# Performance work log

Measured on AMD Instinct MI355X. Metric: run time of the kernel, lower is better.

Reference implementation:

```python
import jax, jax.numpy as jnp
import numpy as np
import math

EMBED_DIM = 256
NUM_HEADS = 8
NUM_LEVELS = 4
NUM_POINTS = 4
HEAD_DIM = EMBED_DIM // NUM_HEADS
SPATIAL_SHAPES = np.array([[100, 100], [50, 50], [25, 25], [13, 13]], dtype=np.int64)
LEN_V = int((SPATIAL_SHAPES[:, 0] * SPATIAL_SHAPES[:, 1]).sum())  # 13294
BS, LEN_Q = 8, 1024


def _grid_sample_bilinear(img, grid):
    """img: [N, C, H, W]; grid: [N, Hg, Wg, 2] in [-1,1].
    bilinear, padding_mode='zeros', align_corners=False. Returns [N, Hg, Wg, C]."""
    N, C, H, W = img.shape
    x = (grid[..., 0] + 1.0) * (W * 0.5) - 0.5
    y = (grid[..., 1] + 1.0) * (H * 0.5) - 0.5
    x0 = jnp.floor(x)
    y0 = jnp.floor(y)
    x1 = x0 + 1.0
    y1 = y0 + 1.0
    wx1 = x - x0
    wx0 = 1.0 - wx1
    wy1 = y - y0
    wy0 = 1.0 - wy1
    b = jnp.arange(N)[:, None, None]

    def gather(yi, xi):
        valid = (yi >= 0) & (yi <= H - 1) & (xi >= 0) & (xi <= W - 1)
        yc = jnp.clip(yi, 0, H - 1).astype(jnp.int32)
        xc = jnp.clip(xi, 0, W - 1).astype(jnp.int32)
        v = img[b, :, yc, xc]  # [N, Hg, Wg, C]
        return v * valid[..., None].astype(img.dtype)

    out = (gather(y0, x0) * (wy0 * wx0)[..., None]
           + gather(y0, x1) * (wy0 * wx1)[..., None]
           + gather(y1, x0) * (wy1 * wx0)[..., None]
           + gather(y1, x1) * (wy1 * wx1)[..., None])
    return out


def _offset_bias_init():
    # Faithful to _reset_parameters: per-head directional grid init for offsets bias.
    thetas = np.arange(NUM_HEADS, dtype=np.float32) * (2.0 * math.pi / NUM_HEADS)
    g = np.stack([np.cos(thetas), np.sin(thetas)], -1)
    g = g / np.abs(g).max(-1, keepdims=True)
    g = np.tile(g.reshape(NUM_HEADS, 1, 1, 2), (1, NUM_LEVELS, NUM_POINTS, 1))
    g = g * np.arange(1, NUM_POINTS + 1, dtype=np.float32).reshape(1, 1, -1, 1)
    return jnp.asarray(g.reshape(-1))


def setup_inputs() -> dict:
    key = jax.random.key(0)
    ks = jax.random.split(key, 8)
    TP = NUM_HEADS * NUM_LEVELS * NUM_POINTS  # 128

    def xavier(k, fan_in, fan_out):
        lim = math.sqrt(6.0 / (fan_in + fan_out))
        return jax.random.uniform(k, (fan_in, fan_out), jnp.float32, -lim, lim)

    return {
        "query": jax.random.normal(ks[0], (BS, LEN_Q, EMBED_DIM), jnp.float32),
        "reference_points": jax.random.uniform(ks[1], (BS, LEN_Q, NUM_LEVELS, 2), jnp.float32),
        "value": jax.random.normal(ks[2], (BS, LEN_V, EMBED_DIM), jnp.float32),
        "value_spatial_shapes": SPATIAL_SHAPES,
        # small random weights (instead of the zero-init) so the math paths are exercised
        "so_w": 0.01 * jax.random.normal(ks[3], (EMBED_DIM, TP * 2), jnp.float32),
        "so_b": _offset_bias_init(),
        "aw_w": 0.01 * jax.random.normal(ks[4], (EMBED_DIM, TP), jnp.float32),
        "aw_b": jnp.zeros((TP,), jnp.float32),
        "vp_w": xavier(ks[5], EMBED_DIM, EMBED_DIM),
        "vp_b": jnp.zeros((EMBED_DIM,), jnp.float32),
        "op_w": xavier(ks[6], EMBED_DIM, EMBED_DIM),
        "op_b": jnp.zeros((EMBED_DIM,), jnp.float32),
    }


def reference(query, reference_points, value, value_spatial_shapes,
              so_w, so_b, aw_w, aw_b, vp_w, vp_b, op_w, op_b):
    shapes = np.asarray(value_spatial_shapes)  # static python ints
    bs, len_q, D = query.shape
    H, L, P, hd = NUM_HEADS, NUM_LEVELS, NUM_POINTS, HEAD_DIM

    v = value @ vp_w + vp_b                              # [bs, len_v, D]
    v = v.reshape(bs, -1, H, hd)                         # [bs, len_v, H, hd]

    so = (query @ so_w + so_b).reshape(bs, len_q, H, L, P, 2)
    aw = (query @ aw_w + aw_b).reshape(bs, len_q, H, L * P)
    aw = jax.nn.softmax(aw, axis=-1).reshape(bs, len_q, H, L, P)

    # reference_points last dim == 2 branch: normalize offsets by (w, h) per level
    norm = jnp.asarray(shapes[:, ::-1].copy(), dtype=query.dtype).reshape(1, 1, 1, L, 1, 2)
    loc = reference_points.reshape(bs, len_q, 1, L, 1, 2) + so / norm
    grids = 2.0 * loc - 1.0                              # [bs, len_q, H, L, P, 2]
    grids = grids.transpose(0, 2, 1, 3, 4, 5).reshape(bs * H, len_q, L, P, 2)

    samples = []
    start = 0
    for lvl in range(L):
        h, w = int(shapes[lvl, 0]), int(shapes[lvl, 1])
        vl = v[:, start:start + h * w]                   # [bs, hw, H, hd]
        start += h * w
        img = vl.transpose(0, 2, 3, 1).reshape(bs * H, hd, h, w)
        s = _grid_sample_bilinear(img, grids[:, :, lvl])  # [bs*H, len_q, P, hd]
        samples.append(s)
    samp = jnp.stack(samples, axis=2)                    # [bs*H, len_q, L, P, hd]

    w_ = aw.transpose(0, 2, 1, 3, 4).reshape(bs * H, len_q, L, P)
    out = jnp.einsum('nqlpd,nqlp->nqd', samp, w_)        # [bs*H, len_q, hd]
    out = out.reshape(bs, H, len_q, hd).transpose(0, 2, 1, 3).reshape(bs, len_q, D)
    return out @ op_w + op_b
```

## Files before the change

kernel.cpp:

```cpp
#include <hip/hip_runtime.h>
#include <math.h>

#define BSZ 8
#define LQ  1024
#define LV  13294
#define NH  8
#define HD  32
#define VM  (BSZ * LV)

typedef __attribute__((ext_vector_type(8))) short bf16x8;
typedef __attribute__((ext_vector_type(8))) unsigned short u16x8;
typedef __attribute__((ext_vector_type(4))) float f32x4;

__device__ static inline unsigned short f2bf(float f) {
    unsigned int u = __float_as_uint(f);
    unsigned int r = (u + 0x7FFFu + ((u >> 16) & 1u)) >> 16;
    return (unsigned short)r;
}
__device__ static inline float bf2f(unsigned short s) {
    return __uint_as_float(((unsigned int)s) << 16);
}

__global__ __launch_bounds__(256) void wconv_kernel(
    const float* __restrict__ w, unsigned short* __restrict__ wT)
{
    const int n = blockIdx.x;
    const int k = threadIdx.x;
    wT[n * 256 + k] = f2bf(w[k * 256 + n]);
}

__global__ __launch_bounds__(256, 2) void vproj_mfma_kernel(
    const float* __restrict__ A,
    const unsigned short* __restrict__ wT,
    const float* __restrict__ bias,
    unsigned short* __restrict__ v)
{
    __shared__ __align__(16) unsigned short Asb[64 * 256];

    const int tid  = threadIdx.x;
    const int w    = tid >> 6;
    const int lane = tid & 63;
    const int mrow = lane & 15;
    const int quad = lane >> 4;
    const int m0   = blockIdx.x * 64;

    bf16x8 wf[4][8];
#pragma unroll
    for (int j = 0; j < 4; ++j) {
        const int n = w * 64 + j * 16 + mrow;
#pragma unroll
        for (int kc = 0; kc < 8; ++kc)
            wf[j][kc] = *(const bf16x8*)(const void*)(wT + (size_t)n * 256 + kc * 32 + quad * 8);
    }
    float bj[4];
#pragma unroll
    for (int j = 0; j < 4; ++j) bj[j] = bias[w * 64 + j * 16 + mrow];

    {
        const int m  = tid >> 2;
        const int kq = tid & 3;
        const int gm = m0 + m;
        const float* ap = A + (size_t)gm * 256 + kq * 64;
        unsigned short* lrow = &Asb[m * 256];
#pragma unroll
        for (int u = 0; u < 8; ++u) {
            const int c  = kq * 8 + u;
            const int cp = c ^ (m & 31);
            u16x8 b8 = (u16x8)0;
            if (gm < VM) {
                const float4 f0 = *(const float4*)(ap + u * 8);
                const float4 f1 = *(const float4*)(ap + u * 8 + 4);
                b8[0] = f2bf(f0.x); b8[1] = f2bf(f0.y);
                b8[2] = f2bf(f0.z); b8[3] = f2bf(f0.w);
                b8[4] = f2bf(f1.x); b8[5] = f2bf(f1.y);
                b8[6] = f2bf(f1.z); b8[7] = f2bf(f1.w);
            }
            *(u16x8*)(lrow + cp * 8) = b8;
        }
    }
    __syncthreads();

    f32x4 acc[4][4];
#pragma unroll
    for (int i = 0; i < 4; ++i)
#pragma unroll
        for (int j = 0; j < 4; ++j) acc[i][j] = (f32x4)0.f;

#pragma unroll
    for (int kc = 0; kc < 8; ++kc) {
        bf16x8 af[4];
#pragma unroll
        for (int i = 0; i < 4; ++i) {
            const int mr = i * 16 + mrow;
            const int c  = kc * 4 + quad;
            const int cp = c ^ (mr & 31);
            af[i] = *(const bf16x8*)(const void*)&Asb[mr * 256 + cp * 8];
        }
#pragma unroll
        for (int i = 0; i < 4; ++i)
#pragma unroll
            for (int j = 0; j < 4; ++j)
                acc[i][j] = __builtin_amdgcn_mfma_f32_16x16x32_bf16(
                    af[i], wf[j][kc], acc[i][j], 0, 0, 0);
    }

#pragma unroll
    for (int i = 0; i < 4; ++i) {
#pragma unroll
        for (int r = 0; r < 4; ++r) {
            const int gm = m0 + i * 16 + quad * 4 + r;
            if (gm >= VM) continue;
            const unsigned int b   = (unsigned int)gm / (unsigned int)LV;
            const unsigned int pix = (unsigned int)gm - b * (unsigned int)LV;
#pragma unroll
            for (int j = 0; j < 4; ++j) {
                const int gn = w * 64 + j * 16 + mrow;
                const int h = gn >> 5, c = gn & 31;
                v[(((size_t)(b * NH + h)) * LV + pix) * HD + c] =
                    f2bf(acc[i][j][r] + bj[j]);
            }
        }
    }
}

__global__ __launch_bounds__(256) void qproj_kernel(
    const float* __restrict__ A,
    const float* __restrict__ so_w, const float* __restrict__ so_b,
    const float* __restrict__ aw_w, const float* __restrict__ aw_b,
    float* __restrict__ so_raw, float* __restrict__ aw_raw)
{
    __shared__ float As[16][68];
    __shared__ float Ws[16][68];

    const int tid = threadIdx.x;
    const int tx = tid & 15, ty = tid >> 4;
    const int m0 = blockIdx.y * 64;
    const int n0g = blockIdx.x * 64;

    const float* W; const float* bias; float* C; int N, n0;
    if (n0g < 256) { W = so_w; bias = so_b; C = so_raw; N = 256; n0 = n0g; }
    else           { W = aw_w; bias = aw_b; C = aw_raw; N = 128; n0 = n0g - 256; }

    const int ra = tid >> 2;
    const int ka = (tid & 3) << 2;
    const int rw = tid >> 4;
    const int cw = (tid & 15) << 2;

    float acc[4][4];
#pragma unroll
    for (int i = 0; i < 4; ++i)
#pragma unroll
        for (int j = 0; j < 4; ++j) acc[i][j] = 0.f;

    for (int k0 = 0; k0 < 256; k0 += 16) {
        const float4 av = *(const float4*)(A + (size_t)(m0 + ra) * 256 + (k0 + ka));
        As[ka + 0][ra] = av.x;
        As[ka + 1][ra] = av.y;
        As[ka + 2][ra] = av.z;
        As[ka + 3][ra] = av.w;
        *(float4*)&Ws[rw][cw] =
            *(const float4*)(W + (size_t)(k0 + rw) * N + (n0 + cw));
        __syncthreads();
#pragma unroll
        for (int k = 0; k < 16; ++k) {
            const float4 a4 = *(const float4*)&As[k][ty << 2];
            const float4 b4 = *(const float4*)&Ws[k][tx << 2];
            const float aa[4] = {a4.x, a4.y, a4.z, a4.w};
            const float bb[4] = {b4.x, b4.y, b4.z, b4.w};
#pragma unroll
            for (int i = 0; i < 4; ++i)
#pragma unroll
                for (int j = 0; j < 4; ++j)
                    acc[i][j] = fmaf(aa[i], bb[j], acc[i][j]);
        }
        __syncthreads();
    }

#pragma unroll
    for (int i = 0; i < 4; ++i) {
        const int row = m0 + (ty << 2) + i;
#pragma unroll
        for (int j = 0; j < 4; ++j) {
            const int col = n0 + (tx << 2) + j;
            C[(size_t)row * N + col] = acc[i][j] + bias[col];
        }
    }
}

__global__ __launch_bounds__(256) void sgemm_kernel(
    const float* __restrict__ A, const float* __restrict__ W,
    const float* __restrict__ bias, float* __restrict__ C)
{
    __shared__ float As[16][68];
    __shared__ float Ws[16][68];

    const int tid = threadIdx.x;
    const int tx = tid & 15, ty = tid >> 4;
    const int m0 = blockIdx.y * 64;
    const int n0 = blockIdx.x * 64;

    const int ra = tid >> 2;
    const int ka = (tid & 3) << 2;
    const int rw = tid >> 4;
    const int cw = (tid & 15) << 2;

    float acc[4][4];
#pragma unroll
    for (int i = 0; i < 4; ++i)
#pragma unroll
        for (int j = 0; j < 4; ++j) acc[i][j] = 0.f;

    for (int k0 = 0; k0 < 256; k0 += 16) {
        const float4 av = *(const float4*)(A + (size_t)(m0 + ra) * 256 + (k0 + ka));
        As[ka + 0][ra] = av.x;
        As[ka + 1][ra] = av.y;
        As[ka + 2][ra] = av.z;
        As[ka + 3][ra] = av.w;
        *(float4*)&Ws[rw][cw] =
            *(const float4*)(W + (size_t)(k0 + rw) * 256 + (n0 + cw));
        __syncthreads();
#pragma unroll
        for (int k = 0; k < 16; ++k) {
            const float4 a4 = *(const float4*)&As[k][ty << 2];
            const float4 b4 = *(const float4*)&Ws[k][tx << 2];
            const float aa[4] = {a4.x, a4.y, a4.z, a4.w};
            const float bb[4] = {b4.x, b4.y, b4.z, b4.w};
#pragma unroll
            for (int i = 0; i < 4; ++i)
#pragma unroll
                for (int j = 0; j < 4; ++j)
                    acc[i][j] = fmaf(aa[i], bb[j], acc[i][j]);
        }
        __syncthreads();
    }

#pragma unroll
    for (int i = 0; i < 4; ++i) {
        const int row = m0 + (ty << 2) + i;
#pragma unroll
        for (int j = 0; j < 4; ++j) {
            const int col = n0 + (tx << 2) + j;
            C[(size_t)row * 256 + col] = acc[i][j] + bias[col];
        }
    }
}

__global__ __launch_bounds__(256) void sample_kernel(
    const unsigned short* __restrict__ v,
    const float* __restrict__ so_raw,
    const float* __restrict__ aw_raw,
    const float* __restrict__ refp,
    float* __restrict__ out_head)
{
    __shared__ __align__(16) float wts[512][4];
    __shared__ __align__(16) int   offs[512][4];

    const int blk   = blockIdx.x;
    const int xcd   = blk & 7;
    const int j     = blk >> 3;
    const int bh    = xcd * 8 + (j >> 5);
    const int chunk = j & 31;
    const int h     = bh & 7;
    const int b     = bh >> 3;

    const int t = threadIdx.x;

#pragma unroll
    for (int rep = 0; rep < 2; ++rep) {
        const int s  = t + rep * 256;
        const int qq = s >> 4;
        const int pt = s & 15;
        const int l  = pt >> 2;
        const int p  = pt & 3;
        const int rq = b * LQ + chunk * 32 + qq;

        const int Wl = (l == 0) ? 100 : (l == 1) ? 50 : (l == 2) ? 25 : 13;
        const int st = (l == 0) ? 0 : (l == 1) ? 10000 : (l == 2) ? 12500 : 13125;
        const float invW = (l == 0) ? 0.01f : (l == 1) ? 0.02f : (l == 2) ? 0.04f
                                            : (1.0f / 13.0f);
        const float fw = (float)Wl;

        const float logit = aw_raw[rq * 128 + h * 16 + pt];
        float mx = logit;
#pragma unroll
        for (int d = 1; d < 16; d <<= 1) mx = fmaxf(mx, __shfl_xor(mx, d, 16));
        const float e = expf(logit - mx);
        float sm = e;
#pragma unroll
        for (int d = 1; d < 16; d <<= 1) sm += __shfl_xor(sm, d, 16);
        const float wgt = e / sm;

        const float rx = refp[((size_t)rq * 4 + l) * 2 + 0];
        const float ry = refp[((size_t)rq * 4 + l) * 2 + 1];
        const int soi  = rq * 256 + h * 32 + l * 8 + p * 2;
        const float sx = so_raw[soi];
        const float sy = so_raw[soi + 1];

        const float x = (rx + sx * invW) * fw - 0.5f;
        const float y = (ry + sy * invW) * fw - 0.5f;

        const float xf = floorf(x), yf = floorf(y);
        const int x0 = (int)xf, y0 = (int)yf;
        const float wx1 = x - xf, wx0 = 1.f - wx1;
        const float wy1 = y - yf, wy0 = 1.f - wy1;

        const float vx0 = (x0 >= 0 && x0 < Wl) ? 1.f : 0.f;
        const float vx1 = (x0 + 1 >= 0 && x0 + 1 < Wl) ? 1.f : 0.f;
        const float vy0 = (y0 >= 0 && y0 < Wl) ? 1.f : 0.f;
        const float vy1 = (y0 + 1 >= 0 && y0 + 1 < Wl) ? 1.f : 0.f;

        const int xc0 = min(max(x0, 0), Wl - 1);
        const int xc1 = min(max(x0 + 1, 0), Wl - 1);
        const int yc0 = min(max(y0, 0), Wl - 1);
        const int yc1 = min(max(y0 + 1, 0), Wl - 1);

        const int row0 = st + yc0 * Wl;
        const int row1 = st + yc1 * Wl;

        wts[s][0] = wgt * wy0 * wx0 * vy0 * vx0;
        wts[s][1] = wgt * wy0 * wx1 * vy0 * vx1;
        wts[s][2] = wgt * wy1 * wx0 * vy1 * vx0;
        wts[s][3] = wgt * wy1 * wx1 * vy1 * vx1;
        offs[s][0] = (row0 + xc0) * HD;
        offs[s][1] = (row0 + xc1) * HD;
        offs[s][2] = (row1 + xc0) * HD;
        offs[s][3] = (row1 + xc1) * HD;
    }
    __syncthreads();

    const int qq = t >> 3;
    const int ln = t & 7;
    const unsigned short* vb = v + (size_t)bh * (LV * HD) + ln * 4;

    float a0 = 0.f, a1 = 0.f, a2 = 0.f, a3 = 0.f;

#pragma unroll 4
    for (int pt = 0; pt < 16; ++pt) {
        const int s = qq * 16 + pt;
        const float4 w4 = *(const float4*)&wts[s][0];
        const int4   o4 = *(const int4*)&offs[s][0];

        const ushort4 u0 = *(const ushort4*)(vb + o4.x);
        const ushort4 u1 = *(const ushort4*)(vb + o4.y);
        const ushort4 u2 = *(const ushort4*)(vb + o4.z);
        const ushort4 u3 = *(const ushort4*)(vb + o4.w);

        a0 = fmaf(w4.x, bf2f(u0.x), a0);
        a1 = fmaf(w4.x, bf2f(u0.y), a1);
        a2 = fmaf(w4.x, bf2f(u0.z), a2);
        a3 = fmaf(w4.x, bf2f(u0.w), a3);
        a0 = fmaf(w4.y, bf2f(u1.x), a0);
        a1 = fmaf(w4.y, bf2f(u1.y), a1);
        a2 = fmaf(w4.y, bf2f(u1.z), a2);
        a3 = fmaf(w4.y, bf2f(u1.w), a3);
        a0 = fmaf(w4.z, bf2f(u2.x), a0);
        a1 = fmaf(w4.z, bf2f(u2.y), a1);
        a2 = fmaf(w4.z, bf2f(u2.z), a2);
        a3 = fmaf(w4.z, bf2f(u2.w), a3);
        a0 = fmaf(w4.w, bf2f(u3.x), a0);
        a1 = fmaf(w4.w, bf2f(u3.y), a1);
        a2 = fmaf(w4.w, bf2f(u3.z), a2);
        a3 = fmaf(w4.w, bf2f(u3.w), a3);
    }

    const int rq = b * LQ + chunk * 32 + qq;
    float4 o; o.x = a0; o.y = a1; o.z = a2; o.w = a3;
    *(float4*)(out_head + (size_t)rq * 256 + (h << 5) + (ln << 2)) = o;
}

extern "C" void kernel_launch(void* const* d_in, const int* in_sizes, int n_in,
                              void* d_out, int out_size, void* d_ws, size_t ws_size,
                              hipStream_t stream)
{
    const float* query = (const float*)d_in[0];
    const float* refp  = (const float*)d_in[1];
    const float* value = (const float*)d_in[2];
    const float* so_w  = (const float*)d_in[4];
    const float* so_b  = (const float*)d_in[5];
    const float* aw_w  = (const float*)d_in[6];
    const float* aw_b  = (const float*)d_in[7];
    const float* vp_w  = (const float*)d_in[8];
    const float* vp_b  = (const float*)d_in[9];
    const float* op_w  = (const float*)d_in[10];
    const float* op_b  = (const float*)d_in[11];
    float* out = (float*)d_out;

    float* ws = (float*)d_ws;
    size_t off = 0;
    unsigned short* v = (unsigned short*)(ws + off);
    off += (size_t)BSZ * NH * LV * HD / 2;
    unsigned short* wT = (unsigned short*)(ws + off); off += 32768;
    float* so_raw   = ws + off; off += (size_t)BSZ * LQ * 256;
    float* aw_raw   = ws + off; off += (size_t)BSZ * LQ * 128;
    float* out_head = ws + off; off += (size_t)BSZ * LQ * 256;

    wconv_kernel<<<256, 256, 0, stream>>>(vp_w, wT);

    {
        dim3 grid((VM + 63) / 64);
        vproj_mfma_kernel<<<grid, 256, 0, stream>>>(value, wT, vp_b, v);
    }
    {
        dim3 grid(6, BSZ * LQ / 64);
        qproj_kernel<<<grid, 256, 0, stream>>>(query, so_w, so_b, aw_w, aw_b,
                                               so_raw, aw_raw);
    }
    {
        dim3 grid(BSZ * NH * (LQ / 32));
        sample_kernel<<<grid, 256, 0, stream>>>(v, so_raw, aw_raw, refp, out_head);
    }
    {
        dim3 grid(256 / 64, BSZ * LQ / 64);
        sgemm_kernel<<<grid, 256, 0, stream>>>(out_head, op_w, op_b, out);
    }
}
```

Before: 287.2 us.

## Move output projection to bf16 MFMA and stream value projection without LDS

Replaces the fp32 SIMT output-projection GEMM with a bf16 MFMA kernel, and the sampling kernel now writes its per-head output as bf16 to feed it. The value-projection kernel drops its LDS staging, reads fp32 rows directly into registers, converts them to bf16, and swaps the MFMA operands so each lane writes contiguous packed output. Both weight transposes run in a single conversion launch. The aim is to cut FP32 ALU cost and memory traffic, at the cost of extra bf16 rounding in the output path and uncoalesced-looking strided global reads in the value GEMM.

Result: slower. 340.5 us (+18.6%).

```diff
diff --git a/kernel.cpp b/kernel.cpp
--- a/kernel.cpp
+++ b/kernel.cpp
@@ -1,4 +1,5 @@
 #include <hip/hip_runtime.h>
+#include <hip/hip_bf16.h>
 #include <math.h>
 
 #define BSZ 8
@@ -9,7 +10,6 @@
 #define VM  (BSZ * LV)
 
 typedef __attribute__((ext_vector_type(8))) short bf16x8;
-typedef __attribute__((ext_vector_type(8))) unsigned short u16x8;
 typedef __attribute__((ext_vector_type(4))) float f32x4;
 
 __device__ static inline unsigned short f2bf(float f) {
@@ -20,23 +20,29 @@
 __device__ static inline float bf2f(unsigned short s) {
     return __uint_as_float(((unsigned int)s) << 16);
 }
+__device__ static inline unsigned int pk2bf(float a, float b) {
+    __hip_bfloat162 h = __float22bfloat162_rn(make_float2(a, b));
+    return *(unsigned int*)&h;
+}
+
+union BF8 { unsigned int u[4]; bf16x8 v; };
 
 __global__ __launch_bounds__(256) void wconv_kernel(
-    const float* __restrict__ w, unsigned short* __restrict__ wT)
-{
-    const int n = blockIdx.x;
+    const float* __restrict__ w0, const float* __restrict__ w1,
+    unsigned short* __restrict__ t0, unsigned short* __restrict__ t1)
+{
+    const int n = blockIdx.x & 255;
     const int k = threadIdx.x;
-    wT[n * 256 + k] = f2bf(w[k * 256 + n]);
-}
-
-__global__ __launch_bounds__(256, 2) void vproj_mfma_kernel(
+    if (blockIdx.x < 256) t0[n * 256 + k] = f2bf(w0[k * 256 + n]);
+    else                  t1[n * 256 + k] = f2bf(w1[k * 256 + n]);
+}
+
+__global__ __launch_bounds__(512, 2) void vproj_mfma_kernel(
     const float* __restrict__ A,
     const unsigned short* __restrict__ wT,
     const float* __restrict__ bias,
     unsigned short* __restrict__ v)
 {
-    __shared__ __align__(16) unsigned short Asb[64 * 256];
-
     const int tid  = threadIdx.x;
     const int w    = tid >> 6;
     const int lane = tid & 63;
@@ -44,81 +50,126 @@
     const int quad = lane >> 4;
     const int m0   = blockIdx.x * 64;
 
-    bf16x8 wf[4][8];
-#pragma unroll
-    for (int j = 0; j < 4; ++j) {
-        const int n = w * 64 + j * 16 + mrow;
+    bf16x8 wf[2][8];
+#pragma unroll
+    for (int j = 0; j < 2; ++j) {
+        const int n = w * 32 + j * 16 + mrow;
 #pragma unroll
         for (int kc = 0; kc < 8; ++kc)
             wf[j][kc] = *(const bf16x8*)(const void*)(wT + (size_t)n * 256 + kc * 32 + quad * 8);
     }
-    float bj[4];
-#pragma unroll
-    for (int j = 0; j < 4; ++j) bj[j] = bias[w * 64 + j * 16 + mrow];
-
-    {
-        const int m  = tid >> 2;
-        const int kq = tid & 3;
-        const int gm = m0 + m;
-        const float* ap = A + (size_t)gm * 256 + kq * 64;
-        unsigned short* lrow = &Asb[m * 256];
-#pragma unroll
-        for (int u = 0; u < 8; ++u) {
-            const int c  = kq * 8 + u;
-            const int cp = c ^ (m & 31);
-            u16x8 b8 = (u16x8)0;
-            if (gm < VM) {
-                const float4 f0 = *(const float4*)(ap + u * 8);
-                const float4 f1 = *(const float4*)(ap + u * 8 + 4);
-                b8[0] = f2bf(f0.x); b8[1] = f2bf(f0.y);
-                b8[2] = f2bf(f0.z); b8[3] = f2bf(f0.w);
-                b8[4] = f2bf(f1.x); b8[5] = f2bf(f1.y);
-                b8[6] = f2bf(f1.z); b8[7] = f2bf(f1.w);
-            }
-            *(u16x8*)(lrow + cp * 8) = b8;
-        }
-    }
-    __syncthreads();
-
-    f32x4 acc[4][4];
+    float4 bj[2];
+#pragma unroll
+    for (int j = 0; j < 2; ++j)
+        bj[j] = *(const float4*)(bias + w * 32 + j * 16 + quad * 4);
+
+    f32x4 acc[4][2];
 #pragma unroll
     for (int i = 0; i < 4; ++i)
 #pragma unroll
-        for (int j = 0; j < 4; ++j) acc[i][j] = (f32x4)0.f;
+        for (int j = 0; j < 2; ++j) acc[i][j] = (f32x4)0.f;
 
 #pragma unroll
     for (int kc = 0; kc < 8; ++kc) {
-        bf16x8 af[4];
+        bf16x8 vf[4];
 #pragma unroll
         for (int i = 0; i < 4; ++i) {
-            const int mr = i * 16 + mrow;
-            const int c  = kc * 4 + quad;
-            const int cp = c ^ (mr & 31);
-            af[i] = *(const bf16x8*)(const void*)&Asb[mr * 256 + cp * 8];
+            int gm = m0 + i * 16 + mrow;
+            gm = (gm < VM) ? gm : (VM - 1);
+            const float* ap = A + (size_t)gm * 256 + kc * 32 + quad * 8;
+            const float4 f0 = *(const float4*)(ap);
+            const float4 f1 = *(const float4*)(ap + 4);
+            BF8 t;
+            t.u[0] = pk2bf(f0.x, f0.y);
+            t.u[1] = pk2bf(f0.z, f0.w);
+            t.u[2] = pk2bf(f1.x, f1.y);
+            t.u[3] = pk2bf(f1.z, f1.w);
+            vf[i] = t.v;
         }
 #pragma unroll
         for (int i = 0; i < 4; ++i)
 #pragma unroll
-            for (int j = 0; j < 4; ++j)
+            for (int j = 0; j < 2; ++j)
                 acc[i][j] = __builtin_amdgcn_mfma_f32_16x16x32_bf16(
-                    af[i], wf[j][kc], acc[i][j], 0, 0, 0);
+                    wf[j][kc], vf[i], acc[i][j], 0, 0, 0);
     }
 
 #pragma unroll
     for (int i = 0; i < 4; ++i) {
-#pragma unroll
-        for (int r = 0; r < 4; ++r) {
-            const int gm = m0 + i * 16 + quad * 4 + r;
-            if (gm >= VM) continue;
-            const unsigned int b   = (unsigned int)gm / (unsigned int)LV;
-            const unsigned int pix = (unsigned int)gm - b * (unsigned int)LV;
-#pragma unroll
-            for (int j = 0; j < 4; ++j) {
-                const int gn = w * 64 + j * 16 + mrow;
-                const int h = gn >> 5, c = gn & 31;
-                v[(((size_t)(b * NH + h)) * LV + pix) * HD + c] =
-                    f2bf(acc[i][j][r] + bj[j]);
-            }
+        const int gm = m0 + i * 16 + mrow;
+        if (gm >= VM) continue;
+        const unsigned int b   = (unsigned int)gm / (unsigned int)LV;
+        const unsigned int pix = (unsigned int)gm - b * (unsigned int)LV;
+        unsigned short* vp = v + (((size_t)(b * NH + w)) * LV + pix) * HD;
+#pragma unroll
+        for (int j = 0; j < 2; ++j) {
+            uint2 o;
+            o.x = pk2bf(acc[i][j][0] + bj[j].x, acc[i][j][1] + bj[j].y);
+            o.y = pk2bf(acc[i][j][2] + bj[j].z, acc[i][j][3] + bj[j].w);
+            *(uint2*)(vp + j * 16 + quad * 4) = o;
+        }
+    }
+}
+
+__global__ __launch_bounds__(512, 2) void oproj_mfma_kernel(
+    const unsigned short* __restrict__ Ah,
+    const unsigned short* __restrict__ opT,
+    const float* __restrict__ bias,
+    float* __restrict__ out)
+{
+    const int tid  = threadIdx.x;
+    const int w    = tid >> 6;
+    const int lane = tid & 63;
+    const int mrow = lane & 15;
+    const int quad = lane >> 4;
+    const int m0   = blockIdx.x * 32;
+
+    bf16x8 wf[2][8];
+#pragma unroll
+    for (int j = 0; j < 2; ++j) {
+        const int n = w * 32 + j * 16 + mrow;
+#pragma unroll
+        for (int kc = 0; kc < 8; ++kc)
+            wf[j][kc] = *(const bf16x8*)(const void*)(opT + (size_t)n * 256 + kc * 32 + quad * 8);
+    }
+    float4 bj[2];
+#pragma unroll
+    for (int j = 0; j < 2; ++j)
+        bj[j] = *(const float4*)(bias + w * 32 + j * 16 + quad * 4);
+
+    f32x4 acc[2][2];
+#pragma unroll
+    for (int i = 0; i < 2; ++i)
+#pragma unroll
+        for (int j = 0; j < 2; ++j) acc[i][j] = (f32x4)0.f;
+
+#pragma unroll
+    for (int kc = 0; kc < 8; ++kc) {
+        bf16x8 af[2];
+#pragma unroll
+        for (int i = 0; i < 2; ++i) {
+            const int gm = m0 + i * 16 + mrow;
+            af[i] = *(const bf16x8*)(const void*)(Ah + (size_t)gm * 256 + kc * 32 + quad * 8);
+        }
+#pragma unroll
+        for (int i = 0; i < 2; ++i)
+#pragma unroll
+            for (int j = 0; j < 2; ++j)
+                acc[i][j] = __builtin_amdgcn_mfma_f32_16x16x32_bf16(
+                    wf[j][kc], af[i], acc[i][j], 0, 0, 0);
+    }
+
+#pragma unroll
+    for (int i = 0; i < 2; ++i) {
+        const int gm = m0 + i * 16 + mrow;
+#pragma unroll
+        for (int j = 0; j < 2; ++j) {
+            float4 o;
+            o.x = acc[i][j][0] + bj[j].x;
+            o.y = acc[i][j][1] + bj[j].y;
+            o.z = acc[i][j][2] + bj[j].z;
+            o.w = acc[i][j][3] + bj[j].w;
+            *(float4*)(out + (size_t)gm * 256 + w * 32 + j * 16 + quad * 4) = o;
         }
     }
 }
@@ -187,70 +238,12 @@
     }
 }
 
-__global__ __launch_bounds__(256) void sgemm_kernel(
-    const float* __restrict__ A, const float* __restrict__ W,
-    const float* __restrict__ bias, float* __restrict__ C)
-{
-    __shared__ float As[16][68];
-    __shared__ float Ws[16][68];
-
-    const int tid = threadIdx.x;
-    const int tx = tid & 15, ty = tid >> 4;
-    const int m0 = blockIdx.y * 64;
-    const int n0 = blockIdx.x * 64;
-
-    const int ra = tid >> 2;
-    const int ka = (tid & 3) << 2;
-    const int rw = tid >> 4;
-    const int cw = (tid & 15) << 2;
-
-    float acc[4][4];
-#pragma unroll
-    for (int i = 0; i < 4; ++i)
-#pragma unroll
-        for (int j = 0; j < 4; ++j) acc[i][j] = 0.f;
-
-    for (int k0 = 0; k0 < 256; k0 += 16) {
-        const float4 av = *(const float4*)(A + (size_t)(m0 + ra) * 256 + (k0 + ka));
-        As[ka + 0][ra] = av.x;
-        As[ka + 1][ra] = av.y;
-        As[ka + 2][ra] = av.z;
-        As[ka + 3][ra] = av.w;
-        *(float4*)&Ws[rw][cw] =
-            *(const float4*)(W + (size_t)(k0 + rw) * 256 + (n0 + cw));
-        __syncthreads();
-#pragma unroll
-        for (int k = 0; k < 16; ++k) {
-            const float4 a4 = *(const float4*)&As[k][ty << 2];
-            const float4 b4 = *(const float4*)&Ws[k][tx << 2];
-            const float aa[4] = {a4.x, a4.y, a4.z, a4.w};
-            const float bb[4] = {b4.x, b4.y, b4.z, b4.w};
-#pragma unroll
-            for (int i = 0; i < 4; ++i)
-#pragma unroll
-                for (int j = 0; j < 4; ++j)
-                    acc[i][j] = fmaf(aa[i], bb[j], acc[i][j]);
-        }
-        __syncthreads();
-    }
-
-#pragma unroll
-    for (int i = 0; i < 4; ++i) {
-        const int row = m0 + (ty << 2) + i;
-#pragma unroll
-        for (int j = 0; j < 4; ++j) {
-            const int col = n0 + (tx << 2) + j;
-            C[(size_t)row * 256 + col] = acc[i][j] + bias[col];
-        }
-    }
-}
-
 __global__ __launch_bounds__(256) void sample_kernel(
     const unsigned short* __restrict__ v,
     const float* __restrict__ so_raw,
     const float* __restrict__ aw_raw,
     const float* __restrict__ refp,
-    float* __restrict__ out_head)
+    unsigned short* __restrict__ out_head)
 {
     __shared__ __align__(16) float wts[512][4];
     __shared__ __align__(16) int   offs[512][4];
@@ -364,8 +357,10 @@
     }
 
     const int rq = b * LQ + chunk * 32 + qq;
-    float4 o; o.x = a0; o.y = a1; o.z = a2; o.w = a3;
-    *(float4*)(out_head + (size_t)rq * 256 + (h << 5) + (ln << 2)) = o;
+    uint2 o;
+    o.x = pk2bf(a0, a1);
+    o.y = pk2bf(a2, a3);
+    *(uint2*)(out_head + (size_t)rq * 256 + (h << 5) + (ln << 2)) = o;
 }
 
 extern "C" void kernel_launch(void* const* d_in, const int* in_sizes, int n_in,
@@ -389,28 +384,24 @@
     size_t off = 0;
     unsigned short* v = (unsigned short*)(ws + off);
     off += (size_t)BSZ * NH * LV * HD / 2;
-    unsigned short* wT = (unsigned short*)(ws + off); off += 32768;
-    float* so_raw   = ws + off; off += (size_t)BSZ * LQ * 256;
-    float* aw_raw   = ws + off; off += (size_t)BSZ * LQ * 128;
-    float* out_head = ws + off; off += (size_t)BSZ * LQ * 256;
-
-    wconv_kernel<<<256, 256, 0, stream>>>(vp_w, wT);
-
-    {
-        dim3 grid((VM + 63) / 64);
-        vproj_mfma_kernel<<<grid, 256, 0, stream>>>(value, wT, vp_b, v);
-    }
+    unsigned short* wTv = (unsigned short*)(ws + off); off += 32768;
+    unsigned short* wTo = (unsigned short*)(ws + off); off += 32768;
+    float* so_raw = ws + off; off += (size_t)BSZ * LQ * 256;
+    float* aw_raw = ws + off; off += (size_t)BSZ * LQ * 128;
+    unsigned short* out_head = (unsigned short*)(ws + off);
+    off += (size_t)BSZ * LQ * 256 / 2;
+
+    wconv_kernel<<<512, 256, 0, stream>>>(vp_w, op_w, wTv, wTo);
+
+    vproj_mfma_kernel<<<(VM + 63) / 64, 512, 0, stream>>>(value, wTv, vp_b, v);
+
     {
         dim3 grid(6, BSZ * LQ / 64);
         qproj_kernel<<<grid, 256, 0, stream>>>(query, so_w, so_b, aw_w, aw_b,
                                                so_raw, aw_raw);
     }
-    {
-        dim3 grid(BSZ * NH * (LQ / 32));
-        sample_kernel<<<grid, 256, 0, stream>>>(v, so_raw, aw_raw, refp, out_head);
-    }
-    {
-        dim3 grid(256 / 64, BSZ * LQ / 64);
-        sgemm_kernel<<<grid, 256, 0, stream>>>(out_head, op_w, op_b, out);
-    }
-}
+    sample_kernel<<<BSZ * NH * (LQ / 32), 256, 0, stream>>>(
+        v, so_raw, aw_raw, refp, out_head);
+
+    oproj_mfma_kernel<<<BSZ * LQ / 32, 512, 0, stream>>>(out_head, wTo, op_b, out);
+}
```
